# Kernel tuning notes

Measured on AMD Instinct MI355X. Metric: run time of the kernel, lower is better.

## Reference

```python
import jax, jax.numpy as jnp
import numpy as np

EPS = 1e-12  # F.normalize default eps (denominator = max(norm, eps))


def setup_inputs() -> dict:
    key = jax.random.key(0)
    ks = jax.random.split(key, 8)
    B, FIN, H, W = 4, 256, 64, 64
    N_MEM, SQ = 64, 16           # sqrt_fin = fin**0.5
    POS_CH = 2                    # PosEncoding concatenates one coord channel per dim
    CIN = FIN + POS_CH
    QK = N_MEM * SQ               # 1024
    # PosEncoding buffer: normalized coordinate grid in [-1, 1], shape [2, H, W]
    ys = jnp.linspace(-1.0, 1.0, H, dtype=jnp.float32)
    xs = jnp.linspace(-1.0, 1.0, W, dtype=jnp.float32)
    gy, gx = jnp.meshgrid(ys, xs, indexing='ij')
    pos = jnp.stack([gy, gx], axis=0)
    s = 0.02
    return {
        'x':    jax.random.normal(ks[0], (B, FIN, H, W), jnp.float32),
        'pos':  pos,
        'wq':   jax.random.normal(ks[1], (QK, CIN), jnp.float32) * s,
        'bq':   jnp.zeros((QK,), jnp.float32),
        'wk':   jax.random.normal(ks[2], (QK, CIN), jnp.float32) * s,
        'bk':   jnp.zeros((QK,), jnp.float32),
        'v':    jax.random.normal(ks[3], (N_MEM, FIN), jnp.float32) * s,
        'wout': jax.random.normal(ks[4], (FIN, FIN), jnp.float32) * s,
        'bout': jnp.zeros((FIN,), jnp.float32),
    }


def reference(x, pos, wq, bq, wk, bk, v, wout, bout):
    B, C, H, W = x.shape
    S = H * W
    n_mem, fin = v.shape
    sq = wq.shape[0] // n_mem
    # PosEncoding: concat coordinate channels
    posb = jnp.broadcast_to(pos[None], (B,) + pos.shape)
    xp = jnp.concatenate([x, posb], axis=1).reshape(B, C + pos.shape[0], S)
    # 1x1 conv projections (channel GEMMs)
    q = jnp.einsum('oc,bcs->bos', wq, xp) + bq[None, :, None]  # [B, n_mem*sq, S]
    k = jnp.einsum('oc,bcs->bos', wk, xp) + bk[None, :, None]
    q = q.reshape(B, n_mem, sq, S).transpose(0, 3, 1, 2)  # [B,S,m,sq]
    k = k.reshape(B, n_mem, sq, S).transpose(0, 3, 2, 1)  # [B,S,sq,m]
    # F.normalize: q over last dim (sqrt_fin), k over dim=1 (sqrt_fin)
    qn = q / jnp.maximum(jnp.linalg.norm(q, axis=-1, keepdims=True), EPS)
    kn = k / jnp.maximum(jnp.linalg.norm(k, axis=2, keepdims=True), EPS)
    # attn[b,s,m,n] = qn . kn ; dropout is identity in eval mode.
    # mean over memory slots m commutes with (attn @ v), so fuse:
    attn_mean = jnp.einsum('bsk,bskn->bsn', qn.mean(axis=2), kn)  # [B,S,n_mem]
    mem = attn_mean @ v                                            # [B,S,fin]
    mem = mem.transpose(0, 2, 1).reshape(B, fin, H, W)
    out = jnp.einsum('of,bfhw->bohw', wout, mem) + bout[None, :, None, None]
    return x + out
```

## Files before the change

### kernel.cpp

```cpp
#include <hip/hip_runtime.h>
#include <stdint.h>

#define EPSN 1e-12f

typedef float f32x16 __attribute__((ext_vector_type(16)));
typedef float f32x4 __attribute__((ext_vector_type(4)));
typedef __bf16 bf16x8 __attribute__((ext_vector_type(8)));
typedef unsigned short u16x4 __attribute__((ext_vector_type(4)));

__device__ __forceinline__ unsigned short f2bf(float f) {
  union { float f; unsigned int u; } v; v.f = f;
  unsigned int u = v.u + 0x7FFFu + ((v.u >> 16) & 1u);
  return (unsigned short)(u >> 16);
}
__device__ __forceinline__ float bf2f(unsigned short h) {
  union { float f; unsigned int u; } v; v.u = ((unsigned int)h) << 16;
  return v.f;
}

#define NKS 17
#define WQF_OFF 0
#define WKF_OFF (32 * NKS * 64 * 8)
#define WVP_OFF (2 * 32 * NKS * 64 * 8)

__global__ __launch_bounds__(256) void prep_kernel(
    const float* __restrict__ wq, const float* __restrict__ bq,
    const float* __restrict__ wk, const float* __restrict__ bk,
    const float* __restrict__ v, const float* __restrict__ wout,
    unsigned short* __restrict__ wsp) {
  int bid = blockIdx.x;
  if (bid < 512) {
    int isK = bid >= 256;
    int ob = (bid & 255) * 4;
    const float* w = isK ? wk : wq;
    const float* bb = isK ? bk : bq;
    unsigned short* dst = wsp + (isK ? WKF_OFF : WQF_OFF);
    for (int i = threadIdx.x; i < 4 * 129; i += 256) {
      int r = i / 129, q = i - r * 129;
      int o = ob + r, k = q * 2;
      float2 w2 = *(const float2*)(w + o * 258 + k);
      int g = o >> 5, col = o & 31;
      int ks = k >> 4, hi = (k >> 3) & 1, j = k & 7;
      uint32_t pk = (uint32_t)f2bf(w2.x) | ((uint32_t)f2bf(w2.y) << 16);
      *(uint32_t*)(dst + (((g * NKS + ks) * 64 + hi * 32 + col) << 3) + j) = pk;
    }
    for (int i = threadIdx.x; i < 4 * 14; i += 256) {
      int r = i / 14, kk = 258 + (i - r * 14);
      int o = ob + r;
      int g = o >> 5, col = o & 31;
      int ks = kk >> 4, hi = (kk >> 3) & 1, j = kk & 7;
      dst[(((g * NKS + ks) * 64 + hi * 32 + col) << 3) + j] =
          (kk == 258) ? f2bf(bb[o]) : (unsigned short)0;
    }
  } else {
    int idx = (bid - 512) * 256 + threadIdx.x;
    int fc = idx & 15, m = (idx >> 4) & 63, o = idx >> 10;
    const f32x4* wo = (const f32x4*)(wout + o * 256 + fc * 16);
    const f32x4* vm = (const f32x4*)(v + m * 256 + fc * 16);
    float s = 0.f;
#pragma unroll
    for (int f = 0; f < 4; ++f) {
      f32x4 a = wo[f], bvv = vm[f];
      s += a[0]*bvv[0] + a[1]*bvv[1] + a[2]*bvv[2] + a[3]*bvv[3];
    }
    s += __shfl_xor(s, 1, 64);
    s += __shfl_xor(s, 2, 64);
    s += __shfl_xor(s, 4, 64);
    s += __shfl_xor(s, 8, 64);
    if (fc == 0) wsp[WVP_OFF + o * 64 + m] = f2bf(s);
  }
}

#define PXB 64
#define KP 296
#define QS 66
#define AT 72

__global__ __launch_bounds__(1024, 4) void fused_kernel(
    const float* __restrict__ x, const float* __restrict__ pos,
    const unsigned short* __restrict__ wsp, const float* __restrict__ bout,
    float* __restrict__ out) {
  __shared__ __align__(16) unsigned short xp[PXB * KP];
  __shared__ __align__(16) float qbarL[16 * QS];
  __shared__ __align__(16) unsigned short attnM[PXB * AT];
  __shared__ float boutL[256];

  const int tid = threadIdx.x;
  const int lane = tid & 63;
  const int wid = __builtin_amdgcn_readfirstlane(tid >> 6);
  const int px = lane & 31, q2 = lane >> 5;
  const int P0 = blockIdx.x * PXB;
  const int b = P0 >> 12, s0 = P0 & 4095;

  const int wtoff = (2 * wid) * NKS * 512 + lane * 8;
  const unsigned short* wqf = wsp + WQF_OFF + wtoff;
  const unsigned short* wkf = wsp + WKF_OFF + wtoff;

  const int kbase = wid;

  bf16x8 ring0[3], ring1[3];
#define RING_FILL(WB) do {                                                \
    _Pragma("unroll")                                                     \
    for (int s = 0; s < 3; ++s) {                                         \
      int kp = kbase + s; if (kp >= NKS) kp -= NKS;                       \
      ring0[s] = *(const bf16x8*)((WB) + kp * 512);                       \
      ring1[s] = *(const bf16x8*)((WB) + NKS * 512 + kp * 512);           \
    }                                                                     \
  } while (0)

  RING_FILL(wqf);

  uint32_t* xp32 = (uint32_t*)xp;
  {
    const float* xrow = x + b * 256 * 4096 + s0;
    f32x4 lo[2], hi[2];
#pragma unroll
    for (int it = 0; it < 2; ++it) {
      int idx = tid + it * 1024;
      int g = idx & 15, dcol = idx >> 4;
      lo[it] = __builtin_nontemporal_load(
          (const f32x4*)(xrow + (2 * dcol) * 4096 + 4 * g));
      hi[it] = __builtin_nontemporal_load(
          (const f32x4*)(xrow + (2 * dcol + 1) * 4096 + 4 * g));
    }
#pragma unroll
    for (int it = 0; it < 2; ++it) {
      int idx = tid + it * 1024;
      int g = idx & 15, dcol = idx >> 4;
#pragma unroll
      for (int j = 0; j < 4; ++j) {
        int pp = 4 * g + j;
        xp32[pp * 148 + dcol] =
            (uint32_t)f2bf(lo[it][j]) | ((uint32_t)f2bf(hi[it][j]) << 16);
      }
    }
    if (tid < 512) {
      int pp = tid & 63, dcol = 128 + (tid >> 6);
      float t0 = 0.f, t1 = 0.f;
      if (dcol == 128) { t0 = pos[s0 + pp]; t1 = pos[4096 + s0 + pp]; }
      else if (dcol == 129) { t0 = 1.0f; }
      xp32[pp * 148 + dcol] = (uint32_t)f2bf(t0) | ((uint32_t)f2bf(t1) << 16);
    }
  }
  if (tid < 256) boutL[tid] = bout[tid];
  for (int i = tid; i < 16 * QS; i += 1024) qbarL[i] = 0.f;
  __syncthreads();

#define PHASE(WB) do {                                                    \
    _Pragma("unroll")                                                     \
    for (int i = 0; i < NKS; ++i) {                                       \
      int ks = kbase + i; if (ks >= NKS) ks -= NKS;                       \
      bf16x8 _A0 = ring0[i % 3], _A1 = ring1[i % 3];                      \
      if (i + 3 < NKS) {                                                  \
        int kp = ks + 3; if (kp >= NKS) kp -= NKS;                        \
        ring0[i % 3] = *(const bf16x8*)((WB) + kp * 512);                 \
        ring1[i % 3] = *(const bf16x8*)((WB) + NKS * 512 + kp * 512);     \
      }                                                                   \
      const int boff = ks * 16 + q2 * 8;                                  \
      bf16x8 _b0 = *(const bf16x8*)&xp[px * KP + boff];                   \
      bf16x8 _b1 = *(const bf16x8*)&xp[(32 + px) * KP + boff];            \
      acc00 = __builtin_amdgcn_mfma_f32_32x32x16_bf16(_A0, _b0, acc00, 0, 0, 0); \
      acc01 = __builtin_amdgcn_mfma_f32_32x32x16_bf16(_A0, _b1, acc01, 0, 0, 0); \
      acc10 = __builtin_amdgcn_mfma_f32_32x32x16_bf16(_A1, _b0, acc10, 0, 0, 0); \
      acc11 = __builtin_amdgcn_mfma_f32_32x32x16_bf16(_A1, _b1, acc11, 0, 0, 0); \
    }                                                                     \
  } while (0)

  f32x16 acc00 = (f32x16)0.f, acc01 = (f32x16)0.f,
         acc10 = (f32x16)0.f, acc11 = (f32x16)0.f;
  PHASE(wqf);

  RING_FILL(wkf);

  {
    float qsum[2][8];
#pragma unroll
    for (int nt = 0; nt < 2; ++nt)
#pragma unroll
      for (int r = 0; r < 8; ++r) qsum[nt][r] = 0.f;
#pragma unroll
    for (int ot = 0; ot < 2; ++ot) {
#pragma unroll
      for (int nt = 0; nt < 2; ++nt) {
        const f32x16 a = ot ? (nt ? acc11 : acc10) : (nt ? acc01 : acc00);
        float s20 = 0.f, s21 = 0.f;
#pragma unroll
        for (int r = 0; r < 8; ++r) {
          s20 = fmaf(a[r], a[r], s20);
          s21 = fmaf(a[r + 8], a[r + 8], s21);
        }
        s20 += __shfl_xor(s20, 32, 64);
        s21 += __shfl_xor(s21, 32, 64);
        float i0 = 1.0f / fmaxf(sqrtf(s20), EPSN);
        float i1 = 1.0f / fmaxf(sqrtf(s21), EPSN);
#pragma unroll
        for (int r = 0; r < 8; ++r) qsum[nt][r] += a[r] * i0 + a[r + 8] * i1;
      }
    }
#pragma unroll
    for (int nt = 0; nt < 2; ++nt)
#pragma unroll
      for (int r = 0; r < 8; ++r) {
        int j = (r & 3) + ((r >> 2) << 3) + (q2 << 2);
        atomicAdd(&qbarL[j * QS + nt * 32 + px], qsum[nt][r] * (1.0f / 64.0f));
      }
  }

  acc00 = (f32x16)0.f; acc01 = (f32x16)0.f;
  acc10 = (f32x16)0.f; acc11 = (f32x16)0.f;
  PHASE(wkf);
  __syncthreads();

  {
    float qb[2][8];
#pragma unroll
    for (int nt = 0; nt < 2; ++nt)
#pragma unroll
      for (int r = 0; r < 8; ++r) {
        int j = (r & 3) + ((r >> 2) << 3) + (q2 << 2);
        qb[nt][r] = qbarL[j * QS + nt * 32 + px];
      }
#pragma unroll
    for (int ot = 0; ot < 2; ++ot) {
#pragma unroll
      for (int nt = 0; nt < 2; ++nt) {
        const f32x16 a = ot ? (nt ? acc11 : acc10) : (nt ? acc01 : acc00);
        float s20 = 0.f, s21 = 0.f, sp0 = 0.f, sp1 = 0.f;
#pragma unroll
        for (int r = 0; r < 8; ++r) {
          s20 = fmaf(a[r], a[r], s20);         sp0 = fmaf(qb[nt][r], a[r], sp0);
          s21 = fmaf(a[r + 8], a[r + 8], s21); sp1 = fmaf(qb[nt][r], a[r + 8], sp1);
        }
        s20 += __shfl_xor(s20, 32, 64);
        s21 += __shfl_xor(s21, 32, 64);
        sp0 += __shfl_xor(sp0, 32, 64);
        sp1 += __shfl_xor(sp1, 32, 64);
        if (q2 == 0) {
          int m0 = wid * 4 + ot * 2;
          attnM[(nt * 32 + px) * AT + m0]     = f2bf(sp0 / fmaxf(sqrtf(s20), EPSN));
          attnM[(nt * 32 + px) * AT + m0 + 1] = f2bf(sp1 / fmaxf(sqrtf(s21), EPSN));
        }
      }
    }
  }
  __syncthreads();

  {
    const int otile = wid >> 1, pxt = wid & 1;
    f32x16 e = (f32x16)0.f;
    const unsigned short* wv = wsp + WVP_OFF + (otile * 32 + px) * 64 + q2 * 8;
    const unsigned short* ab = &attnM[(pxt * 32 + px) * AT + q2 * 8];
#pragma unroll
    for (int ks = 0; ks < 4; ++ks) {
      bf16x8 av = *(const bf16x8*)(wv + ks * 16);
      bf16x8 bv = *(const bf16x8*)(ab + ks * 16);
      e = __builtin_amdgcn_mfma_f32_32x32x16_bf16(av, bv, e, 0, 0, 0);
    }
    const int p = pxt * 32 + px;
    const unsigned short* xl = &xp[p * KP + otile * 32 + (q2 << 2)];
#pragma unroll
    for (int rq = 0; rq < 4; ++rq) {
      u16x4 xq = *(const u16x4*)(xl + 8 * rq);
#pragma unroll
      for (int j = 0; j < 4; ++j) {
        const int r = rq * 4 + j;
        const int o = otile * 32 + j + (rq << 3) + (q2 << 2);
        const int gi = (b * 256 + o) * 4096 + s0 + p;
        __builtin_nontemporal_store(bf2f(xq[j]) + boutL[o] + e[r], &out[gi]);
      }
    }
  }
#undef PHASE
#undef RING_FILL
}

extern "C" void kernel_launch(void* const* d_in, const int* in_sizes, int n_in,
                              void* d_out, int out_size, void* d_ws, size_t ws_size,
                              hipStream_t stream) {
  const float* x    = (const float*)d_in[0];
  const float* pos  = (const float*)d_in[1];
  const float* wq   = (const float*)d_in[2];
  const float* bq   = (const float*)d_in[3];
  const float* wk   = (const float*)d_in[4];
  const float* bk   = (const float*)d_in[5];
  const float* v    = (const float*)d_in[6];
  const float* wout = (const float*)d_in[7];
  const float* bout = (const float*)d_in[8];
  float* out = (float*)d_out;
  unsigned short* wsp = (unsigned short*)d_ws;

  hipLaunchKernelGGL(prep_kernel, dim3(1536), dim3(256), 0, stream,
                     wq, bq, wk, bk, v, wout, wsp);
  hipLaunchKernelGGL(fused_kernel, dim3(256), dim3(1024), 0, stream,
                     x, pos, wsp, bout, out);
}
```

Before: 127.6 us.

## Replace 3-deep weight ring with rolled 1-ahead prefetch and MFMA priority

```diff
diff --git a/kernel.cpp b/kernel.cpp
--- a/kernel.cpp
+++ b/kernel.cpp
@@ -96,20 +96,6 @@
   const unsigned short* wqf = wsp + WQF_OFF + wtoff;
   const unsigned short* wkf = wsp + WKF_OFF + wtoff;
 
-  const int kbase = wid;
-
-  bf16x8 ring0[3], ring1[3];
-#define RING_FILL(WB) do {                                                \
-    _Pragma("unroll")                                                     \
-    for (int s = 0; s < 3; ++s) {                                         \
-      int kp = kbase + s; if (kp >= NKS) kp -= NKS;                       \
-      ring0[s] = *(const bf16x8*)((WB) + kp * 512);                       \
-      ring1[s] = *(const bf16x8*)((WB) + NKS * 512 + kp * 512);           \
-    }                                                                     \
-  } while (0)
-
-  RING_FILL(wqf);
-
   uint32_t* xp32 = (uint32_t*)xp;
   {
     const float* xrow = x + b * 256 * 4096 + s0;
@@ -147,30 +133,39 @@
   __syncthreads();
 
 #define PHASE(WB) do {                                                    \
-    _Pragma("unroll")                                                     \
-    for (int i = 0; i < NKS; ++i) {                                       \
-      int ks = kbase + i; if (ks >= NKS) ks -= NKS;                       \
-      bf16x8 _A0 = ring0[i % 3], _A1 = ring1[i % 3];                      \
-      if (i + 3 < NKS) {                                                  \
-        int kp = ks + 3; if (kp >= NKS) kp -= NKS;                        \
-        ring0[i % 3] = *(const bf16x8*)((WB) + kp * 512);                 \
-        ring1[i % 3] = *(const bf16x8*)((WB) + NKS * 512 + kp * 512);     \
-      }                                                                   \
-      const int boff = ks * 16 + q2 * 8;                                  \
-      bf16x8 _b0 = *(const bf16x8*)&xp[px * KP + boff];                   \
-      bf16x8 _b1 = *(const bf16x8*)&xp[(32 + px) * KP + boff];            \
-      acc00 = __builtin_amdgcn_mfma_f32_32x32x16_bf16(_A0, _b0, acc00, 0, 0, 0); \
-      acc01 = __builtin_amdgcn_mfma_f32_32x32x16_bf16(_A0, _b1, acc01, 0, 0, 0); \
-      acc10 = __builtin_amdgcn_mfma_f32_32x32x16_bf16(_A1, _b0, acc10, 0, 0, 0); \
-      acc11 = __builtin_amdgcn_mfma_f32_32x32x16_bf16(_A1, _b1, acc11, 0, 0, 0); \
+    const unsigned short* _p0 = (WB);                                     \
+    const unsigned short* _p1 = (WB) + NKS * 512;                         \
+    const unsigned short* _bp0 = &xp[px * KP + q2 * 8];                   \
+    const unsigned short* _bp1 = &xp[(32 + px) * KP + q2 * 8];            \
+    bf16x8 _A0c = *(const bf16x8*)_p0;                                    \
+    bf16x8 _A1c = *(const bf16x8*)_p1;                                    \
+    _Pragma("unroll 1")                                                   \
+    for (int i = 0; i < NKS - 1; ++i) {                                   \
+      bf16x8 _A0n = *(const bf16x8*)(_p0 + (i + 1) * 512);                \
+      bf16x8 _A1n = *(const bf16x8*)(_p1 + (i + 1) * 512);                \
+      bf16x8 _b0 = *(const bf16x8*)(_bp0 + i * 16);                       \
+      bf16x8 _b1 = *(const bf16x8*)(_bp1 + i * 16);                       \
+      __builtin_amdgcn_s_setprio(1);                                      \
+      acc00 = __builtin_amdgcn_mfma_f32_32x32x16_bf16(_A0c, _b0, acc00, 0, 0, 0); \
+      acc01 = __builtin_amdgcn_mfma_f32_32x32x16_bf16(_A0c, _b1, acc01, 0, 0, 0); \
+      acc10 = __builtin_amdgcn_mfma_f32_32x32x16_bf16(_A1c, _b0, acc10, 0, 0, 0); \
+      acc11 = __builtin_amdgcn_mfma_f32_32x32x16_bf16(_A1c, _b1, acc11, 0, 0, 0); \
+      __builtin_amdgcn_s_setprio(0);                                      \
+      _A0c = _A0n; _A1c = _A1n;                                           \
+    }                                                                     \
+    {                                                                     \
+      bf16x8 _b0 = *(const bf16x8*)(_bp0 + (NKS - 1) * 16);               \
+      bf16x8 _b1 = *(const bf16x8*)(_bp1 + (NKS - 1) * 16);               \
+      acc00 = __builtin_amdgcn_mfma_f32_32x32x16_bf16(_A0c, _b0, acc00, 0, 0, 0); \
+      acc01 = __builtin_amdgcn_mfma_f32_32x32x16_bf16(_A0c, _b1, acc01, 0, 0, 0); \
+      acc10 = __builtin_amdgcn_mfma_f32_32x32x16_bf16(_A1c, _b0, acc10, 0, 0, 0); \
+      acc11 = __builtin_amdgcn_mfma_f32_32x32x16_bf16(_A1c, _b1, acc11, 0, 0, 0); \
     }                                                                     \
   } while (0)
 
   f32x16 acc00 = (f32x16)0.f, acc01 = (f32x16)0.f,
          acc10 = (f32x16)0.f, acc11 = (f32x16)0.f;
   PHASE(wqf);
-
-  RING_FILL(wkf);
 
   {
     float qsum[2][8];
@@ -271,7 +266,6 @@
     }
   }
 #undef PHASE
-#undef RING_FILL
 }
 
 extern "C" void kernel_launch(void* const* d_in, const int* in_sizes, int n_in,
```

Result: no change. 127.8 us (+0.2%).
